# Performance work log

Measured on AMD Instinct MI355X. Metric: run time of the kernel, lower is better.

Reference implementation:

```python
import jax, jax.numpy as jnp
import numpy as np

N = 100_000      # nodes (10kb Hi-C bins)
E = 3_200_000    # edges (avg degree 32)
IN = 6           # histone-mark features
HID1 = 6
HID2 = 30
HEADS = 4
NEG_SLOPE = 0.2  # PyG GATConv default LeakyReLU slope


def setup_inputs() -> dict:
    key = jax.random.key(0)
    ks = jax.random.split(key, 16)
    def glorot(k, shape, fan_in):
        return (jax.random.normal(k, shape, jnp.float32) / np.float32(np.sqrt(fan_in)))
    x = jax.random.normal(ks[0], (N, IN), jnp.float32)
    edge_index = jax.random.randint(ks[1], (2, E), 0, N, dtype=jnp.int32)
    edge_attr = jax.random.uniform(ks[2], (E,), jnp.float32)  # ignored (edge_dim=None)
    # GATConv 1: IN -> HID1, HEADS, concat=True
    w1 = glorot(ks[3], (IN, HEADS * HID1), IN)
    att_src1 = glorot(ks[4], (HEADS, HID1), HID1)
    att_dst1 = glorot(ks[5], (HEADS, HID1), HID1)
    b1 = jnp.zeros((HEADS * HID1,), jnp.float32)
    # GATConv 2: HEADS*HID1 -> HID2, HEADS, concat=False (head mean)
    w2 = glorot(ks[6], (HEADS * HID1, HEADS * HID2), HEADS * HID1)
    att_src2 = glorot(ks[7], (HEADS, HID2), HID2)
    att_dst2 = glorot(ks[8], (HEADS, HID2), HID2)
    b2 = jnp.zeros((HID2,), jnp.float32)
    # MLP head
    ffw1 = glorot(ks[9], (HID2, HID2 // 2), HID2)
    ffb1 = jnp.zeros((HID2 // 2,), jnp.float32)
    ffw2 = glorot(ks[10], (HID2 // 2, 2), HID2 // 2)
    ffb2 = jnp.zeros((2,), jnp.float32)
    return {"x": x, "edge_index": edge_index, "edge_attr": edge_attr,
            "w1": w1, "att_src1": att_src1, "att_dst1": att_dst1, "b1": b1,
            "w2": w2, "att_src2": att_src2, "att_dst2": att_dst2, "b2": b2,
            "ffw1": ffw1, "ffb1": ffb1, "ffw2": ffw2, "ffb2": ffb2}


def _leaky(z):
    return jnp.where(z > 0, z, NEG_SLOPE * z)


def _gat_conv(x, src, dst, W, a_src, a_dst, b, heads, ch, concat):
    n = x.shape[0]
    h = (x @ W).reshape(n, heads, ch)                       # [N,H,C]
    asrc = jnp.einsum('nhc,hc->nh', h, a_src)               # [N,H]
    adst = jnp.einsum('nhc,hc->nh', h, a_dst)               # [N,H]
    e = _leaky(asrc[src] + adst[dst])                       # [E,H]
    # stable segment softmax over incoming edges of each dst node
    m = jax.ops.segment_max(e, dst, num_segments=n)
    e = jnp.exp(e - m[dst])
    denom = jax.ops.segment_sum(e, dst, num_segments=n)
    alpha = e / (denom[dst] + 1e-16)                        # [E,H]
    msg = h[src] * alpha[:, :, None]                        # [E,H,C]
    out = jax.ops.segment_sum(msg, dst, num_segments=n)     # [N,H,C]
    out = out.reshape(n, heads * ch) if concat else out.mean(axis=1)
    return out + b


def reference(x, edge_index, edge_attr, w1, att_src1, att_dst1, b1,
              w2, att_src2, att_dst2, b2, ffw1, ffb1, ffw2, ffb2):
    n = x.shape[0]
    # PyG GATConv add_self_loops=True (edge_attr ignored: edge_dim=None)
    loops = jnp.arange(n, dtype=edge_index.dtype)
    ei = jnp.concatenate([edge_index, jnp.stack([loops, loops])], axis=1)
    src, dst = ei[0], ei[1]
    h = jax.nn.relu(_gat_conv(x, src, dst, w1, att_src1, att_dst1, b1, HEADS, HID1, True))
    h = jax.nn.relu(_gat_conv(h, src, dst, w2, att_src2, att_dst2, b2, HEADS, HID2, False))
    # dropout(p=0.5) is identity at inference
    h = jax.nn.relu(h @ ffw1 + ffb1)
    return h @ ffw2 + ffb2
```

## Files before the change

kernel.cpp:

```cpp
#include <hip/hip_runtime.h>
#include <hip/hip_fp16.h>

#define NEG_SLOPE 0.2f
#define NPB 128
#define MAXB 1024

__device__ __forceinline__ unsigned pk2(float a, float b) {
    __half2 h = __floats2half2_rn(a, b);
    return *(unsigned*)&h;
}
__device__ __forceinline__ float exh(unsigned u, int hi) {
    __half2 h = *(__half2*)&u;
    return hi ? __high2float(h) : __low2float(h);
}

__global__ void p0_count(const int* __restrict__ dst, int* __restrict__ bcnt,
                         int E, int nbuck)
{
    __shared__ int hist[MAXB];
    for (int b = threadIdx.x; b < nbuck; b += blockDim.x) hist[b] = 0;
    __syncthreads();
    int tile = blockIdx.x * 4096;
    int cnt = min(4096, E - tile);
    for (int k = threadIdx.x; k < cnt; k += blockDim.x)
        atomicAdd(&hist[dst[tile + k] >> 7], 1);
    __syncthreads();
    for (int b = threadIdx.x; b < nbuck; b += blockDim.x) {
        int v = hist[b];
        if (v) atomicAdd(&bcnt[b], v);
    }
}

__global__ void p1_scan(const int* __restrict__ bcnt, int* __restrict__ bbase,
                        int* __restrict__ bcur, int nbuck)
{
    __shared__ int sm[MAXB];
    int t = threadIdx.x;
    int v = (t < nbuck) ? bcnt[t] : 0;
    sm[t] = v;
    __syncthreads();
    for (int off = 1; off < MAXB; off <<= 1) {
        int x = (t >= off) ? sm[t - off] : 0;
        __syncthreads();
        sm[t] += x;
        __syncthreads();
    }
    if (t < nbuck) { int e = sm[t] - v; bbase[t] = e; bcur[t] = e; }
}

__global__ void p2_scatter(const int* __restrict__ src, const int* __restrict__ dst,
                           int* __restrict__ bcur, int* __restrict__ ebuf,
                           int E, int nbuck)
{
    __shared__ int hist[MAXB];
    __shared__ int base[MAXB];
    __shared__ int pk[4096];
    __shared__ unsigned short pb[4096];
    for (int b = threadIdx.x; b < nbuck; b += blockDim.x) hist[b] = 0;
    __syncthreads();
    int tile = blockIdx.x * 4096;
    int cnt = min(4096, E - tile);
    for (int k = threadIdx.x; k < cnt; k += blockDim.x) {
        int i = tile + k;
        int d = dst[i];
        int b = d >> 7;
        pk[k] = (src[i] << 7) | (d & 127);
        pb[k] = (unsigned short)b;
        atomicAdd(&hist[b], 1);
    }
    __syncthreads();
    for (int b = threadIdx.x; b < nbuck; b += blockDim.x) {
        int v = hist[b];
        base[b] = v ? atomicAdd(&bcur[b], v) : 0;
        hist[b] = 0;
    }
    __syncthreads();
    for (int k = threadIdx.x; k < cnt; k += blockDim.x) {
        int b = pb[k];
        int r = atomicAdd(&hist[b], 1);
        ebuf[base[b] + r] = pk[k];
    }
}

__global__ void p3_sort(const int* __restrict__ bbase, const int* __restrict__ bcnt,
                        const int* __restrict__ ebuf,
                        int* __restrict__ rowp, int* __restrict__ deg,
                        int* __restrict__ esrc, int N)
{
    __shared__ int hist[NPB];
    __shared__ int ls[NPB];
    int b = blockIdx.x;
    int n0 = b * NPB;
    if (threadIdx.x < NPB) hist[threadIdx.x] = 0;
    __syncthreads();
    int es = bbase[b], ec = bcnt[b];
    for (int k = threadIdx.x; k < ec; k += blockDim.x)
        atomicAdd(&hist[ebuf[es + k] & 127], 1);
    __syncthreads();
    if (threadIdx.x < NPB) ls[threadIdx.x] = hist[threadIdx.x];
    __syncthreads();
    for (int off = 1; off < NPB; off <<= 1) {
        int v = 0;
        if (threadIdx.x < NPB && threadIdx.x >= off) v = ls[threadIdx.x - off];
        __syncthreads();
        if (threadIdx.x < NPB) ls[threadIdx.x] += v;
        __syncthreads();
    }
    if (threadIdx.x < NPB) {
        int ex = ls[threadIdx.x] - hist[threadIdx.x];
        ls[threadIdx.x] = ex;
        int n = n0 + threadIdx.x;
        if (n < N) { rowp[n] = es + ex; deg[n] = hist[threadIdx.x]; }
        hist[threadIdx.x] = 0;
    }
    __syncthreads();
    for (int k = threadIdx.x; k < ec; k += blockDim.x) {
        int v = ebuf[es + k];
        int ln = v & 127;
        int r = atomicAdd(&hist[ln], 1);
        esrc[es + ls[ln] + r] = v >> 7;
    }
}

__global__ void k_fold(const float* __restrict__ W1,
                       const float* __restrict__ s1, const float* __restrict__ d1,
                       const float* __restrict__ W2,
                       const float* __restrict__ s2, const float* __restrict__ d2,
                       float* __restrict__ fold)
{
    int t = threadIdx.x;
    if (t < 24) {
        int h = t / 6, k = t % 6;
        float v = 0.f;
        for (int c = 0; c < 6; ++c) v += W1[k * 24 + h * 6 + c] * s1[h * 6 + c];
        fold[t] = v;
    } else if (t < 48) {
        int u = t - 24, h = u / 6, k = u % 6;
        float v = 0.f;
        for (int c = 0; c < 6; ++c) v += W1[k * 24 + h * 6 + c] * d1[h * 6 + c];
        fold[t] = v;
    } else if (t < 144) {
        int u = t - 48, h = u / 24, k = u % 24;
        float v = 0.f;
        for (int c = 0; c < 30; ++c) v += W2[k * 120 + h * 30 + c] * s2[h * 30 + c];
        fold[t] = v;
    } else if (t < 240) {
        int u = t - 144, h = u / 24, k = u % 24;
        float v = 0.f;
        for (int c = 0; c < 30; ++c) v += W2[k * 120 + h * 30 + c] * d2[h * 30 + c];
        fold[t] = v;
    }
}

__global__ void k1_row(const float* __restrict__ x,
                       const float* __restrict__ fold,
                       float* __restrict__ row1, float* __restrict__ ad1, int N)
{
    int n = blockIdx.x * blockDim.x + threadIdx.x;
    if (n >= N) return;
    float xv[6];
#pragma unroll
    for (int k = 0; k < 6; ++k) xv[k] = x[n * 6 + k];
    float as[4], ad[4];
#pragma unroll
    for (int h = 0; h < 4; ++h) {
        float a = 0.f, d = 0.f;
#pragma unroll
        for (int k = 0; k < 6; ++k) {
            a += xv[k] * fold[h * 6 + k];
            d += xv[k] * fold[24 + h * 6 + k];
        }
        as[h] = a; ad[h] = d;
        ad1[n * 4 + h] = d;
    }
    uint4 u0, u1;
    u0.x = pk2(as[0], as[1]);
    u0.y = pk2(as[2], as[3]);
    u0.z = __float_as_uint(xv[0]);
    u0.w = __float_as_uint(xv[1]);
    u1.x = __float_as_uint(xv[2]);
    u1.y = __float_as_uint(xv[3]);
    u1.z = __float_as_uint(xv[4]);
    u1.w = __float_as_uint(xv[5]);
    uint4* rp = (uint4*)row1 + (size_t)n * 2;
    rp[0] = u0; rp[1] = u1;
}

__global__ void k_gather1(const int* __restrict__ rowp, const int* __restrict__ deg,
                          const int* __restrict__ esrc,
                          const float* __restrict__ row1,
                          const float* __restrict__ ad1,
                          const float* __restrict__ W1, const float* __restrict__ b1,
                          const float* __restrict__ fold,
                          float* __restrict__ rowA, float* __restrict__ rowB,
                          float* __restrict__ ad2, int N)
{
    int t = blockIdx.x * blockDim.x + threadIdx.x;
    int n = t >> 3;
    if (n >= N) return;
    int o = t & 7;
    int h = o & 3;
    int half = o >> 2;
    float adn = ad1[n * 4 + h];
    const uint4* R = (const uint4*)row1;

    float acc[6] = {0.f, 0.f, 0.f, 0.f, 0.f, 0.f};
    float den = 0.f;
    if (half == 0) {
        uint4 u0 = R[(size_t)n * 2], u1 = R[(size_t)n * 2 + 1];
        float asn = exh((h < 2) ? u0.x : u0.y, h & 1);
        float e0 = asn + adn;
        e0 = e0 > 0.f ? e0 : NEG_SLOPE * e0;
        float w = expf(e0);
        den = w;
        acc[0] = w * __uint_as_float(u0.z);
        acc[1] = w * __uint_as_float(u0.w);
        acc[2] = w * __uint_as_float(u1.x);
        acc[3] = w * __uint_as_float(u1.y);
        acc[4] = w * __uint_as_float(u1.z);
        acc[5] = w * __uint_as_float(u1.w);
    }
    int start = rowp[n], cnt = deg[n];
    for (int k = half; k < cnt; k += 2) {
        int s = esrc[start + k];
        uint4 u0 = R[(size_t)s * 2], u1 = R[(size_t)s * 2 + 1];
        float as = exh((h < 2) ? u0.x : u0.y, h & 1);
        float e = as + adn;
        e = e > 0.f ? e : NEG_SLOPE * e;
        float w = expf(e);
        den += w;
        acc[0] += w * __uint_as_float(u0.z);
        acc[1] += w * __uint_as_float(u0.w);
        acc[2] += w * __uint_as_float(u1.x);
        acc[3] += w * __uint_as_float(u1.y);
        acc[4] += w * __uint_as_float(u1.z);
        acc[5] += w * __uint_as_float(u1.w);
    }
    den += __shfl_xor(den, 4);
#pragma unroll
    for (int k = 0; k < 6; ++k) acc[k] += __shfl_xor(acc[k], 4);

    float inv = 1.f / (den + 1e-16f);
    float m[6];
#pragma unroll
    for (int k = 0; k < 6; ++k) m[k] = acc[k] * inv;

    float gc[6];
#pragma unroll
    for (int c = 0; c < 6; ++c) {
        float v = b1[h * 6 + c];
#pragma unroll
        for (int k = 0; k < 6; ++k) v += m[k] * W1[k * 24 + h * 6 + c];
        gc[c] = v > 0.f ? v : 0.f;
    }
    float pas[4], pad[4];
#pragma unroll
    for (int hh = 0; hh < 4; ++hh) {
        float a = 0.f, d = 0.f;
#pragma unroll
        for (int c = 0; c < 6; ++c) {
            a += gc[c] * fold[48 + hh * 24 + h * 6 + c];
            d += gc[c] * fold[144 + hh * 24 + h * 6 + c];
        }
        pas[hh] = a; pad[hh] = d;
    }
#pragma unroll
    for (int hh = 0; hh < 4; ++hh) {
        pas[hh] += __shfl_xor(pas[hh], 1);
        pas[hh] += __shfl_xor(pas[hh], 2);
        pad[hh] += __shfl_xor(pad[hh], 1);
        pad[hh] += __shfl_xor(pad[hh], 2);
    }
    if (half == 0) {
        unsigned* rp = (unsigned*)((h < 2) ? rowA : rowB) + (size_t)n * 8;
        if ((h & 1) == 0) {
            rp[0] = pk2(pas[0], pas[1]);
            rp[1] = pk2(pas[2], pas[3]);
        }
        int gb = 2 + (h & 1) * 3;
        rp[gb + 0] = pk2(gc[0], gc[1]);
        rp[gb + 1] = pk2(gc[2], gc[3]);
        rp[gb + 2] = pk2(gc[4], gc[5]);
        ad2[n * 4 + h] = pad[h];
    }
}

__global__ void k_g2a(const int* __restrict__ rowp, const int* __restrict__ deg,
                      const int* __restrict__ esrc,
                      const float* __restrict__ rowA, const float* __restrict__ ad2,
                      const float* __restrict__ W2,
                      float* __restrict__ zA, int N)
{
    int t = blockIdx.x * blockDim.x + threadIdx.x;
    int n = t >> 3;
    if (n >= N) return;
    int o = t & 7;
    int h = o & 3;
    int half = o >> 2;
    float adn = ad2[n * 4 + h];
    const uint4* R = (const uint4*)rowA;

    float acc[12];
#pragma unroll
    for (int k = 0; k < 12; ++k) acc[k] = 0.f;
    float den = 0.f;

    if (half == 0) {
        uint4 u0 = R[(size_t)n * 2], u1 = R[(size_t)n * 2 + 1];
        float as = exh((h < 2) ? u0.x : u0.y, h & 1);
        float e = as + adn; e = e > 0.f ? e : NEG_SLOPE * e;
        float w = expf(e);
        den = w;
        float2 g0 = __half22float2(*(__half2*)&u0.z);
        float2 g1 = __half22float2(*(__half2*)&u0.w);
        float2 g2 = __half22float2(*(__half2*)&u1.x);
        float2 g3 = __half22float2(*(__half2*)&u1.y);
        float2 g4 = __half22float2(*(__half2*)&u1.z);
        float2 g5 = __half22float2(*(__half2*)&u1.w);
        acc[0]=w*g0.x; acc[1]=w*g0.y; acc[2]=w*g1.x; acc[3]=w*g1.y;
        acc[4]=w*g2.x; acc[5]=w*g2.y; acc[6]=w*g3.x; acc[7]=w*g3.y;
        acc[8]=w*g4.x; acc[9]=w*g4.y; acc[10]=w*g5.x; acc[11]=w*g5.y;
    }
    int start = rowp[n], cnt = deg[n];
    for (int k = half; k < cnt; k += 2) {
        int s = esrc[start + k];
        uint4 u0 = R[(size_t)s * 2], u1 = R[(size_t)s * 2 + 1];
        float as = exh((h < 2) ? u0.x : u0.y, h & 1);
        float e = as + adn; e = e > 0.f ? e : NEG_SLOPE * e;
        float w = expf(e);
        den += w;
        float2 g0 = __half22float2(*(__half2*)&u0.z);
        float2 g1 = __half22float2(*(__half2*)&u0.w);
        float2 g2 = __half22float2(*(__half2*)&u1.x);
        float2 g3 = __half22float2(*(__half2*)&u1.y);
        float2 g4 = __half22float2(*(__half2*)&u1.z);
        float2 g5 = __half22float2(*(__half2*)&u1.w);
        acc[0]+=w*g0.x; acc[1]+=w*g0.y; acc[2]+=w*g1.x; acc[3]+=w*g1.y;
        acc[4]+=w*g2.x; acc[5]+=w*g2.y; acc[6]+=w*g3.x; acc[7]+=w*g3.y;
        acc[8]+=w*g4.x; acc[9]+=w*g4.y; acc[10]+=w*g5.x; acc[11]+=w*g5.y;
    }
    den += __shfl_xor(den, 4);
#pragma unroll
    for (int k = 0; k < 12; ++k) acc[k] += __shfl_xor(acc[k], 4);
    float inv = 1.f / (den + 1e-16f);
#pragma unroll
    for (int k = 0; k < 12; ++k) acc[k] *= inv;

    float vv[15];
#pragma unroll
    for (int cc = 0; cc < 15; ++cc) {
        int c = half * 15 + cc;
        float v = 0.f;
#pragma unroll
        for (int k = 0; k < 12; ++k) v += acc[k] * W2[k * 120 + h * 30 + c];
        v += __shfl_xor(v, 1);
        v += __shfl_xor(v, 2);
        vv[cc] = v;
    }
    if (h == 0) {
#pragma unroll
        for (int cc = 0; cc < 15; ++cc)
            zA[(size_t)n * 30 + half * 15 + cc] = vv[cc];
    }
}

__global__ void k_g2b(const int* __restrict__ rowp, const int* __restrict__ deg,
                      const int* __restrict__ esrc,
                      const float* __restrict__ rowB, const float* __restrict__ ad2,
                      const float* __restrict__ W2, const float* __restrict__ zA,
                      const float* __restrict__ b2,
                      const float* __restrict__ fw1, const float* __restrict__ fb1,
                      const float* __restrict__ fw2, const float* __restrict__ fb2,
                      float* __restrict__ out, int N)
{
    int t = blockIdx.x * blockDim.x + threadIdx.x;
    int n = t >> 3;
    if (n >= N) return;
    int o = t & 7;
    int h = o & 3;
    int half = o >> 2;
    float adn = ad2[n * 4 + h];
    const uint4* R = (const uint4*)rowB;

    float acc[12];
#pragma unroll
    for (int k = 0; k < 12; ++k) acc[k] = 0.f;
    float den = 0.f;

    if (half == 0) {
        uint4 u0 = R[(size_t)n * 2], u1 = R[(size_t)n * 2 + 1];
        float as = exh((h < 2) ? u0.x : u0.y, h & 1);
        float e = as + adn; e = e > 0.f ? e : NEG_SLOPE * e;
        float w = expf(e);
        den = w;
        float2 g0 = __half22float2(*(__half2*)&u0.z);
        float2 g1 = __half22float2(*(__half2*)&u0.w);
        float2 g2 = __half22float2(*(__half2*)&u1.x);
        float2 g3 = __half22float2(*(__half2*)&u1.y);
        float2 g4 = __half22float2(*(__half2*)&u1.z);
        float2 g5 = __half22float2(*(__half2*)&u1.w);
        acc[0]=w*g0.x; acc[1]=w*g0.y; acc[2]=w*g1.x; acc[3]=w*g1.y;
        acc[4]=w*g2.x; acc[5]=w*g2.y; acc[6]=w*g3.x; acc[7]=w*g3.y;
        acc[8]=w*g4.x; acc[9]=w*g4.y; acc[10]=w*g5.x; acc[11]=w*g5.y;
    }
    int start = rowp[n], cnt = deg[n];
    for (int k = half; k < cnt; k += 2) {
        int s = esrc[start + k];
        uint4 u0 = R[(size_t)s * 2], u1 = R[(size_t)s * 2 + 1];
        float as = exh((h < 2) ? u0.x : u0.y, h & 1);
        float e = as + adn; e = e > 0.f ? e : NEG_SLOPE * e;
        float w = expf(e);
        den += w;
        float2 g0 = __half22float2(*(__half2*)&u0.z);
        float2 g1 = __half22float2(*(__half2*)&u0.w);
        float2 g2 = __half22float2(*(__half2*)&u1.x);
        float2 g3 = __half22float2(*(__half2*)&u1.y);
        float2 g4 = __half22float2(*(__half2*)&u1.z);
        float2 g5 = __half22float2(*(__half2*)&u1.w);
        acc[0]+=w*g0.x; acc[1]+=w*g0.y; acc[2]+=w*g1.x; acc[3]+=w*g1.y;
        acc[4]+=w*g2.x; acc[5]+=w*g2.y; acc[6]+=w*g3.x; acc[7]+=w*g3.y;
        acc[8]+=w*g4.x; acc[9]+=w*g4.y; acc[10]+=w*g5.x; acc[11]+=w*g5.y;
    }
    den += __shfl_xor(den, 4);
#pragma unroll
    for (int k = 0; k < 12; ++k) acc[k] += __shfl_xor(acc[k], 4);
    float inv = 1.f / (den + 1e-16f);
#pragma unroll
    for (int k = 0; k < 12; ++k) acc[k] *= inv;

    float zz[15];
#pragma unroll
    for (int cc = 0; cc < 15; ++cc) {
        int c = half * 15 + cc;
        float v = 0.f;
#pragma unroll
        for (int k = 0; k < 12; ++k) v += acc[k] * W2[(12 + k) * 120 + h * 30 + c];
        v += __shfl_xor(v, 1);
        v += __shfl_xor(v, 2);
        zz[cc] = v;
    }
    float zhi[15];
#pragma unroll
    for (int cc = 0; cc < 15; ++cc) zhi[cc] = __shfl_xor(zz[cc], 4);

    if (o == 0) {
        float z[30];
#pragma unroll
        for (int cc = 0; cc < 15; ++cc) {
            float v0 = 0.25f * (zz[cc] + zA[(size_t)n * 30 + cc]) + b2[cc];
            float v1 = 0.25f * (zhi[cc] + zA[(size_t)n * 30 + 15 + cc]) + b2[15 + cc];
            z[cc]      = v0 > 0.f ? v0 : 0.f;
            z[15 + cc] = v1 > 0.f ? v1 : 0.f;
        }
        float m2[15];
#pragma unroll
        for (int j = 0; j < 15; ++j) {
            float v = fb1[j];
#pragma unroll
            for (int c = 0; c < 30; ++c) v += z[c] * fw1[c * 15 + j];
            m2[j] = v > 0.f ? v : 0.f;
        }
#pragma unroll
        for (int k = 0; k < 2; ++k) {
            float v = fb2[k];
#pragma unroll
            for (int j = 0; j < 15; ++j) v += m2[j] * fw2[j * 2 + k];
            out[(size_t)n * 2 + k] = v;
        }
    }
}

extern "C" void kernel_launch(void* const* d_in, const int* in_sizes, int n_in,
                              void* d_out, int out_size, void* d_ws, size_t ws_size,
                              hipStream_t stream)
{
    const float* x    = (const float*)d_in[0];
    const int*   ei   = (const int*)  d_in[1];
    const float* w1   = (const float*)d_in[3];
    const float* as1w = (const float*)d_in[4];
    const float* ad1w = (const float*)d_in[5];
    const float* b1   = (const float*)d_in[6];
    const float* w2   = (const float*)d_in[7];
    const float* as2w = (const float*)d_in[8];
    const float* ad2w = (const float*)d_in[9];
    const float* b2   = (const float*)d_in[10];
    const float* fw1  = (const float*)d_in[11];
    const float* fb1  = (const float*)d_in[12];
    const float* fw2  = (const float*)d_in[13];
    const float* fb2  = (const float*)d_in[14];

    const int N = in_sizes[0] / 6;
    const int E = in_sizes[1] / 2;
    const int* src = ei;
    const int* dst = ei + E;
    const int nbuck = (N + NPB - 1) / NPB;

    float* ws = (float*)d_ws;
    size_t off = 0;
    float* row1 = ws + off; off += (size_t)N * 8;
    float* rowA = ws + off; off += (size_t)N * 8;
    float* rowB = ws + off; off += (size_t)N * 8;
    float* ad1  = ws + off; off += (size_t)N * 4;
    float* ad2  = ws + off; off += (size_t)N * 4;
    float* zA   = ws + off; off += (size_t)N * 30;
    float* fold = ws + off; off += 256;

    int* iw = (int*)(ws + off);
    size_t ioff = 0;
    int* bcnt  = iw + ioff; ioff += MAXB;
    int* bbase = iw + ioff; ioff += MAXB;
    int* bcur  = iw + ioff; ioff += MAXB;
    int* rowp  = iw + ioff; ioff += N;
    int* deg   = iw + ioff; ioff += N;
    int* ebuf  = iw + ioff; ioff += E;
    int* esrc  = iw + ioff; ioff += E;

    hipMemsetAsync(bcnt, 0, MAXB * sizeof(int), stream);

    const int B = 256;
    const int NB = (N + B - 1) / B;
    const int TB = (E + 4095) / 4096;
    const int OB = ((size_t)N * 8 + B - 1) / B;

    k_fold    <<<1, 256, 0, stream>>>(w1, as1w, ad1w, w2, as2w, ad2w, fold);

    p0_count  <<<TB, B, 0, stream>>>(dst, bcnt, E, nbuck);
    p1_scan   <<<1, MAXB, 0, stream>>>(bcnt, bbase, bcur, nbuck);
    p2_scatter<<<TB, B, 0, stream>>>(src, dst, bcur, ebuf, E, nbuck);
    p3_sort   <<<nbuck, B, 0, stream>>>(bbase, bcnt, ebuf, rowp, deg, esrc, N);

    k1_row    <<<NB, B, 0, stream>>>(x, fold, row1, ad1, N);
    k_gather1 <<<OB, B, 0, stream>>>(rowp, deg, esrc, row1, ad1, w1, b1, fold,
                                     rowA, rowB, ad2, N);

    k_g2a     <<<OB, B, 0, stream>>>(rowp, deg, esrc, rowA, ad2, w2, zA, N);
    k_g2b     <<<OB, B, 0, stream>>>(rowp, deg, esrc, rowB, ad2, w2, zA, b2,
                                     fw1, fb1, fw2, fb2, (float*)d_out, N);
}
```

Before: 395.2 us.

## Fuse split layer-2 gathers into one kernel with unrolled contiguous edge loops

Merges the two half-feature layer-2 gather kernels (rowA/rowB plus a zA intermediate) into one kernel that gathers a 64-byte row per source node, so edge indices and attention terms are read once and the zA round trip goes away. The edge loops in both gather kernels now give each half-thread a contiguous edge range and unroll by four to issue more independent loads. W2 is staged in shared memory. The cost is double the accumulator registers (24 floats), which may lower occupancy, plus a per-block 11KB shared-memory fill.

```diff
diff --git a/kernel.cpp b/kernel.cpp
--- a/kernel.cpp
+++ b/kernel.cpp
@@ -192,7 +192,7 @@
                           const float* __restrict__ ad1,
                           const float* __restrict__ W1, const float* __restrict__ b1,
                           const float* __restrict__ fold,
-                          float* __restrict__ rowA, float* __restrict__ rowB,
+                          float* __restrict__ row2,
                           float* __restrict__ ad2, int N)
 {
     int t = blockIdx.x * blockDim.x + threadIdx.x;
@@ -221,8 +221,38 @@
         acc[5] = w * __uint_as_float(u1.w);
     }
     int start = rowp[n], cnt = deg[n];
-    for (int k = half; k < cnt; k += 2) {
-        int s = esrc[start + k];
+    int c0 = (cnt + 1) >> 1;
+    int lo = start + (half ? c0 : 0);
+    int hi = start + (half ? cnt : c0);
+
+    int k = lo;
+    for (; k + 4 <= hi; k += 4) {
+        int s[4];
+#pragma unroll
+        for (int j = 0; j < 4; ++j) s[j] = esrc[k + j];
+        uint4 a[4], b[4];
+#pragma unroll
+        for (int j = 0; j < 4; ++j) {
+            a[j] = R[(size_t)s[j] * 2];
+            b[j] = R[(size_t)s[j] * 2 + 1];
+        }
+#pragma unroll
+        for (int j = 0; j < 4; ++j) {
+            float as = exh((h < 2) ? a[j].x : a[j].y, h & 1);
+            float e = as + adn;
+            e = e > 0.f ? e : NEG_SLOPE * e;
+            float w = expf(e);
+            den += w;
+            acc[0] += w * __uint_as_float(a[j].z);
+            acc[1] += w * __uint_as_float(a[j].w);
+            acc[2] += w * __uint_as_float(b[j].x);
+            acc[3] += w * __uint_as_float(b[j].y);
+            acc[4] += w * __uint_as_float(b[j].z);
+            acc[5] += w * __uint_as_float(b[j].w);
+        }
+    }
+    for (; k < hi; ++k) {
+        int s = esrc[k];
         uint4 u0 = R[(size_t)s * 2], u1 = R[(size_t)s * 2 + 1];
         float as = exh((h < 2) ? u0.x : u0.y, h & 1);
         float e = as + adn;
@@ -238,19 +268,19 @@
     }
     den += __shfl_xor(den, 4);
 #pragma unroll
-    for (int k = 0; k < 6; ++k) acc[k] += __shfl_xor(acc[k], 4);
+    for (int q = 0; q < 6; ++q) acc[q] += __shfl_xor(acc[q], 4);
 
     float inv = 1.f / (den + 1e-16f);
     float m[6];
 #pragma unroll
-    for (int k = 0; k < 6; ++k) m[k] = acc[k] * inv;
+    for (int q = 0; q < 6; ++q) m[q] = acc[q] * inv;
 
     float gc[6];
 #pragma unroll
     for (int c = 0; c < 6; ++c) {
         float v = b1[h * 6 + c];
 #pragma unroll
-        for (int k = 0; k < 6; ++k) v += m[k] * W1[k * 24 + h * 6 + c];
+        for (int q = 0; q < 6; ++q) v += m[q] * W1[q * 24 + h * 6 + c];
         gc[c] = v > 0.f ? v : 0.f;
     }
     float pas[4], pad[4];
@@ -272,25 +302,31 @@
         pad[hh] += __shfl_xor(pad[hh], 2);
     }
     if (half == 0) {
-        unsigned* rp = (unsigned*)((h < 2) ? rowA : rowB) + (size_t)n * 8;
-        if ((h & 1) == 0) {
+        unsigned* rp = (unsigned*)row2 + (size_t)n * 16;
+        if (h == 0) {
             rp[0] = pk2(pas[0], pas[1]);
             rp[1] = pk2(pas[2], pas[3]);
         }
-        int gb = 2 + (h & 1) * 3;
-        rp[gb + 0] = pk2(gc[0], gc[1]);
-        rp[gb + 1] = pk2(gc[2], gc[3]);
-        rp[gb + 2] = pk2(gc[4], gc[5]);
+        rp[2 + 3 * h + 0] = pk2(gc[0], gc[1]);
+        rp[2 + 3 * h + 1] = pk2(gc[2], gc[3]);
+        rp[2 + 3 * h + 2] = pk2(gc[4], gc[5]);
         ad2[n * 4 + h] = pad[h];
     }
 }
 
-__global__ void k_g2a(const int* __restrict__ rowp, const int* __restrict__ deg,
-                      const int* __restrict__ esrc,
-                      const float* __restrict__ rowA, const float* __restrict__ ad2,
-                      const float* __restrict__ W2,
-                      float* __restrict__ zA, int N)
-{
+__global__ void k_gather2(const int* __restrict__ rowp, const int* __restrict__ deg,
+                          const int* __restrict__ esrc,
+                          const float* __restrict__ row2,
+                          const float* __restrict__ ad2,
+                          const float* __restrict__ W2, const float* __restrict__ b2,
+                          const float* __restrict__ fw1, const float* __restrict__ fb1,
+                          const float* __restrict__ fw2, const float* __restrict__ fb2,
+                          float* __restrict__ out, int N)
+{
+    __shared__ float W2l[24 * 120];
+    for (int i = threadIdx.x; i < 24 * 120; i += blockDim.x) W2l[i] = W2[i];
+    __syncthreads();
+
     int t = blockIdx.x * blockDim.x + threadIdx.x;
     int n = t >> 3;
     if (n >= N) return;
@@ -298,143 +334,97 @@
     int h = o & 3;
     int half = o >> 2;
     float adn = ad2[n * 4 + h];
-    const uint4* R = (const uint4*)rowA;
-
-    float acc[12];
-#pragma unroll
-    for (int k = 0; k < 12; ++k) acc[k] = 0.f;
+    const uint4* R = (const uint4*)row2;
+    const uint2* R2 = (const uint2*)row2;
+
+    float acc[24];
+#pragma unroll
+    for (int q = 0; q < 24; ++q) acc[q] = 0.f;
     float den = 0.f;
 
+#define G2_EDGE(A, B, C, D)                                                   \
+    {                                                                         \
+        float as = exh((h < 2) ? (A).x : (A).y, h & 1);                       \
+        float e = as + adn; e = e > 0.f ? e : NEG_SLOPE * e;                  \
+        float w = expf(e);                                                    \
+        den += w;                                                             \
+        float2 g0 = __half22float2(*(__half2*)&(A).z);                        \
+        float2 g1 = __half22float2(*(__half2*)&(A).w);                        \
+        float2 g2 = __half22float2(*(__half2*)&(B).x);                        \
+        float2 g3 = __half22float2(*(__half2*)&(B).y);                        \
+        float2 g4 = __half22float2(*(__half2*)&(B).z);                        \
+        float2 g5 = __half22float2(*(__half2*)&(B).w);                        \
+        float2 g6 = __half22float2(*(__half2*)&(C).x);                        \
+        float2 g7 = __half22float2(*(__half2*)&(C).y);                        \
+        float2 g8 = __half22float2(*(__half2*)&(C).z);                        \
+        float2 g9 = __half22float2(*(__half2*)&(C).w);                        \
+        float2 gA = __half22float2(*(__half2*)&(D).x);                        \
+        float2 gB = __half22float2(*(__half2*)&(D).y);                        \
+        acc[0] += w * g0.x;  acc[1] += w * g0.y;                              \
+        acc[2] += w * g1.x;  acc[3] += w * g1.y;                              \
+        acc[4] += w * g2.x;  acc[5] += w * g2.y;                              \
+        acc[6] += w * g3.x;  acc[7] += w * g3.y;                              \
+        acc[8] += w * g4.x;  acc[9] += w * g4.y;                              \
+        acc[10] += w * g5.x; acc[11] += w * g5.y;                             \
+        acc[12] += w * g6.x; acc[13] += w * g6.y;                             \
+        acc[14] += w * g7.x; acc[15] += w * g7.y;                             \
+        acc[16] += w * g8.x; acc[17] += w * g8.y;                             \
+        acc[18] += w * g9.x; acc[19] += w * g9.y;                             \
+        acc[20] += w * gA.x; acc[21] += w * gA.y;                             \
+        acc[22] += w * gB.x; acc[23] += w * gB.y;                             \
+    }
+
     if (half == 0) {
-        uint4 u0 = R[(size_t)n * 2], u1 = R[(size_t)n * 2 + 1];
-        float as = exh((h < 2) ? u0.x : u0.y, h & 1);
-        float e = as + adn; e = e > 0.f ? e : NEG_SLOPE * e;
-        float w = expf(e);
-        den = w;
-        float2 g0 = __half22float2(*(__half2*)&u0.z);
-        float2 g1 = __half22float2(*(__half2*)&u0.w);
-        float2 g2 = __half22float2(*(__half2*)&u1.x);
-        float2 g3 = __half22float2(*(__half2*)&u1.y);
-        float2 g4 = __half22float2(*(__half2*)&u1.z);
-        float2 g5 = __half22float2(*(__half2*)&u1.w);
-        acc[0]=w*g0.x; acc[1]=w*g0.y; acc[2]=w*g1.x; acc[3]=w*g1.y;
-        acc[4]=w*g2.x; acc[5]=w*g2.y; acc[6]=w*g3.x; acc[7]=w*g3.y;
-        acc[8]=w*g4.x; acc[9]=w*g4.y; acc[10]=w*g5.x; acc[11]=w*g5.y;
+        uint4 A = R[(size_t)n * 4], B = R[(size_t)n * 4 + 1],
+              C = R[(size_t)n * 4 + 2];
+        uint2 D = R2[(size_t)n * 8 + 6];
+        G2_EDGE(A, B, C, D)
     }
     int start = rowp[n], cnt = deg[n];
-    for (int k = half; k < cnt; k += 2) {
-        int s = esrc[start + k];
-        uint4 u0 = R[(size_t)s * 2], u1 = R[(size_t)s * 2 + 1];
-        float as = exh((h < 2) ? u0.x : u0.y, h & 1);
-        float e = as + adn; e = e > 0.f ? e : NEG_SLOPE * e;
-        float w = expf(e);
-        den += w;
-        float2 g0 = __half22float2(*(__half2*)&u0.z);
-        float2 g1 = __half22float2(*(__half2*)&u0.w);
-        float2 g2 = __half22float2(*(__half2*)&u1.x);
-        float2 g3 = __half22float2(*(__half2*)&u1.y);
-        float2 g4 = __half22float2(*(__half2*)&u1.z);
-        float2 g5 = __half22float2(*(__half2*)&u1.w);
-        acc[0]+=w*g0.x; acc[1]+=w*g0.y; acc[2]+=w*g1.x; acc[3]+=w*g1.y;
-        acc[4]+=w*g2.x; acc[5]+=w*g2.y; acc[6]+=w*g3.x; acc[7]+=w*g3.y;
-        acc[8]+=w*g4.x; acc[9]+=w*g4.y; acc[10]+=w*g5.x; acc[11]+=w*g5.y;
-    }
+    int c0 = (cnt + 1) >> 1;
+    int lo = start + (half ? c0 : 0);
+    int hi = start + (half ? cnt : c0);
+
+    int k = lo;
+    for (; k + 4 <= hi; k += 4) {
+        int s[4];
+#pragma unroll
+        for (int j = 0; j < 4; ++j) s[j] = esrc[k + j];
+        uint4 A[4], B[4], C[4];
+        uint2 D[4];
+#pragma unroll
+        for (int j = 0; j < 4; ++j) {
+            A[j] = R[(size_t)s[j] * 4];
+            B[j] = R[(size_t)s[j] * 4 + 1];
+            C[j] = R[(size_t)s[j] * 4 + 2];
+            D[j] = R2[(size_t)s[j] * 8 + 6];
+        }
+#pragma unroll
+        for (int j = 0; j < 4; ++j) G2_EDGE(A[j], B[j], C[j], D[j])
+    }
+    for (; k < hi; ++k) {
+        int s = esrc[k];
+        uint4 A = R[(size_t)s * 4], B = R[(size_t)s * 4 + 1],
+              C = R[(size_t)s * 4 + 2];
+        uint2 D = R2[(size_t)s * 8 + 6];
+        G2_EDGE(A, B, C, D)
+    }
+#undef G2_EDGE
+
     den += __shfl_xor(den, 4);
 #pragma unroll
-    for (int k = 0; k < 12; ++k) acc[k] += __shfl_xor(acc[k], 4);
+    for (int q = 0; q < 24; ++q) acc[q] += __shfl_xor(acc[q], 4);
     float inv = 1.f / (den + 1e-16f);
 #pragma unroll
-    for (int k = 0; k < 12; ++k) acc[k] *= inv;
-
-    float vv[15];
+    for (int q = 0; q < 24; ++q) acc[q] *= inv;
+
+    float zz[15];
 #pragma unroll
     for (int cc = 0; cc < 15; ++cc) {
         int c = half * 15 + cc;
         float v = 0.f;
 #pragma unroll
-        for (int k = 0; k < 12; ++k) v += acc[k] * W2[k * 120 + h * 30 + c];
-        v += __shfl_xor(v, 1);
-        v += __shfl_xor(v, 2);
-        vv[cc] = v;
-    }
-    if (h == 0) {
-#pragma unroll
-        for (int cc = 0; cc < 15; ++cc)
-            zA[(size_t)n * 30 + half * 15 + cc] = vv[cc];
-    }
-}
-
-__global__ void k_g2b(const int* __restrict__ rowp, const int* __restrict__ deg,
-                      const int* __restrict__ esrc,
-                      const float* __restrict__ rowB, const float* __restrict__ ad2,
-                      const float* __restrict__ W2, const float* __restrict__ zA,
-                      const float* __restrict__ b2,
-                      const float* __restrict__ fw1, const float* __restrict__ fb1,
-                      const float* __restrict__ fw2, const float* __restrict__ fb2,
-                      float* __restrict__ out, int N)
-{
-    int t = blockIdx.x * blockDim.x + threadIdx.x;
-    int n = t >> 3;
-    if (n >= N) return;
-    int o = t & 7;
-    int h = o & 3;
-    int half = o >> 2;
-    float adn = ad2[n * 4 + h];
-    const uint4* R = (const uint4*)rowB;
-
-    float acc[12];
-#pragma unroll
-    for (int k = 0; k < 12; ++k) acc[k] = 0.f;
-    float den = 0.f;
-
-    if (half == 0) {
-        uint4 u0 = R[(size_t)n * 2], u1 = R[(size_t)n * 2 + 1];
-        float as = exh((h < 2) ? u0.x : u0.y, h & 1);
-        float e = as + adn; e = e > 0.f ? e : NEG_SLOPE * e;
-        float w = expf(e);
-        den = w;
-        float2 g0 = __half22float2(*(__half2*)&u0.z);
-        float2 g1 = __half22float2(*(__half2*)&u0.w);
-        float2 g2 = __half22float2(*(__half2*)&u1.x);
-        float2 g3 = __half22float2(*(__half2*)&u1.y);
-        float2 g4 = __half22float2(*(__half2*)&u1.z);
-        float2 g5 = __half22float2(*(__half2*)&u1.w);
-        acc[0]=w*g0.x; acc[1]=w*g0.y; acc[2]=w*g1.x; acc[3]=w*g1.y;
-        acc[4]=w*g2.x; acc[5]=w*g2.y; acc[6]=w*g3.x; acc[7]=w*g3.y;
-        acc[8]=w*g4.x; acc[9]=w*g4.y; acc[10]=w*g5.x; acc[11]=w*g5.y;
-    }
-    int start = rowp[n], cnt = deg[n];
-    for (int k = half; k < cnt; k += 2) {
-        int s = esrc[start + k];
-        uint4 u0 = R[(size_t)s * 2], u1 = R[(size_t)s * 2 + 1];
-        float as = exh((h < 2) ? u0.x : u0.y, h & 1);
-        float e = as + adn; e = e > 0.f ? e : NEG_SLOPE * e;
-        float w = expf(e);
-        den += w;
-        float2 g0 = __half22float2(*(__half2*)&u0.z);
-        float2 g1 = __half22float2(*(__half2*)&u0.w);
-        float2 g2 = __half22float2(*(__half2*)&u1.x);
-        float2 g3 = __half22float2(*(__half2*)&u1.y);
-        float2 g4 = __half22float2(*(__half2*)&u1.z);
-        float2 g5 = __half22float2(*(__half2*)&u1.w);
-        acc[0]+=w*g0.x; acc[1]+=w*g0.y; acc[2]+=w*g1.x; acc[3]+=w*g1.y;
-        acc[4]+=w*g2.x; acc[5]+=w*g2.y; acc[6]+=w*g3.x; acc[7]+=w*g3.y;
-        acc[8]+=w*g4.x; acc[9]+=w*g4.y; acc[10]+=w*g5.x; acc[11]+=w*g5.y;
-    }
-    den += __shfl_xor(den, 4);
-#pragma unroll
-    for (int k = 0; k < 12; ++k) acc[k] += __shfl_xor(acc[k], 4);
-    float inv = 1.f / (den + 1e-16f);
-#pragma unroll
-    for (int k = 0; k < 12; ++k) acc[k] *= inv;
-
-    float zz[15];
-#pragma unroll
-    for (int cc = 0; cc < 15; ++cc) {
-        int c = half * 15 + cc;
-        float v = 0.f;
-#pragma unroll
-        for (int k = 0; k < 12; ++k) v += acc[k] * W2[(12 + k) * 120 + h * 30 + c];
+        for (int q = 0; q < 24; ++q) v += acc[q] * W2l[q * 120 + h * 30 + c];
         v += __shfl_xor(v, 1);
         v += __shfl_xor(v, 2);
         zz[cc] = v;
@@ -447,8 +437,8 @@
         float z[30];
 #pragma unroll
         for (int cc = 0; cc < 15; ++cc) {
-            float v0 = 0.25f * (zz[cc] + zA[(size_t)n * 30 + cc]) + b2[cc];
-            float v1 = 0.25f * (zhi[cc] + zA[(size_t)n * 30 + 15 + cc]) + b2[15 + cc];
+            float v0 = 0.25f * zz[cc] + b2[cc];
+            float v1 = 0.25f * zhi[cc] + b2[15 + cc];
             z[cc]      = v0 > 0.f ? v0 : 0.f;
             z[15 + cc] = v1 > 0.f ? v1 : 0.f;
         }
@@ -461,11 +451,11 @@
             m2[j] = v > 0.f ? v : 0.f;
         }
 #pragma unroll
-        for (int k = 0; k < 2; ++k) {
-            float v = fb2[k];
-#pragma unroll
-            for (int j = 0; j < 15; ++j) v += m2[j] * fw2[j * 2 + k];
-            out[(size_t)n * 2 + k] = v;
+        for (int q = 0; q < 2; ++q) {
+            float v = fb2[q];
+#pragma unroll
+            for (int j = 0; j < 15; ++j) v += m2[j] * fw2[j * 2 + q];
+            out[(size_t)n * 2 + q] = v;
         }
     }
 }
@@ -498,11 +488,9 @@
     float* ws = (float*)d_ws;
     size_t off = 0;
     float* row1 = ws + off; off += (size_t)N * 8;
-    float* rowA = ws + off; off += (size_t)N * 8;
-    float* rowB = ws + off; off += (size_t)N * 8;
+    float* row2 = ws + off; off += (size_t)N * 16;
     float* ad1  = ws + off; off += (size_t)N * 4;
     float* ad2  = ws + off; off += (size_t)N * 4;
-    float* zA   = ws + off; off += (size_t)N * 30;
     float* fold = ws + off; off += 256;
 
     int* iw = (int*)(ws + off);
@@ -531,9 +519,8 @@
 
     k1_row    <<<NB, B, 0, stream>>>(x, fold, row1, ad1, N);
     k_gather1 <<<OB, B, 0, stream>>>(rowp, deg, esrc, row1, ad1, w1, b1, fold,
-                                     rowA, rowB, ad2, N);
-
-    k_g2a     <<<OB, B, 0, stream>>>(rowp, deg, esrc, rowA, ad2, w2, zA, N);
-    k_g2b     <<<OB, B, 0, stream>>>(rowp, deg, esrc, rowB, ad2, w2, zA, b2,
+                                     row2, ad2, N);
+
+    k_gather2 <<<OB, B, 0, stream>>>(rowp, deg, esrc, row2, ad2, w2, b2,
                                      fw1, fb1, fw2, fb2, (float*)d_out, N);
 }
```

Result: no change. 398.3 us (+0.8%).
